# Kernel optimization log

Measured on AMD Instinct MI355X. Metric: run time of the kernel, lower is better.

The kernel has to match this reference:

```python
import jax, jax.numpy as jnp
import numpy as np

B, CIN, H, W = 2, 32, 64, 64
COUT, K, PAD = 32, 3, 1
KK = K * K
PRED_W = COUT * CIN * KK  # 9216 dynamic-weight channels
PRED_OUT = PRED_W + COUT  # + per-pixel bias
EPS = 1e-12


def setup_inputs() -> dict:
    key = jax.random.key(0)
    k1, k2 = jax.random.split(key)
    x = jax.random.normal(k1, (B, CIN, H, W), dtype=jnp.float32)
    # 1x1-conv predictor weights (Conv2d(in_ch, pred_out, 1)), fan-in scaled
    Wp = jax.random.normal(k2, (PRED_OUT, CIN), dtype=jnp.float32) / np.sqrt(CIN).astype(np.float32)
    bp = jnp.zeros((PRED_OUT,), dtype=jnp.float32)
    return {"x": x, "Wp": Wp, "bp": bp}


def _unfold3x3(x):
    # F.unfold with k=3, pad=1, stride=1, dilation=1 -> (B, Cin, 9, L), c slowest then (kh, kw)
    xp = jnp.pad(x, ((0, 0), (0, 0), (PAD, PAD), (PAD, PAD)))
    patches = jnp.stack(
        [xp[:, :, i:i + H, j:j + W] for i in range(K) for j in range(K)], axis=2
    )  # (B, Cin, 9, H, W)
    return patches.reshape(B, CIN, KK, H * W)


def _l2norm(v, axis):
    n = jnp.sqrt(jnp.sum(v * v, axis=axis, keepdims=True))
    return v / jnp.maximum(n, EPS)


def reference(x, Wp, bp):
    L = H * W
    patches = _unfold3x3(x)  # (B, Cin, 9, L)
    # 1x1 conv predictor (stride=1 path -> operates on x directly)
    pred = jnp.einsum('oc,bchw->bohw', Wp, x) + bp[None, :, None, None]  # (B, PRED_OUT, H, W)
    dyn_w = pred[:, :PRED_W].reshape(B, COUT, CIN, KK, L)
    dyn_b = pred[:, PRED_W:].reshape(B, COUT, L)
    # norm_pred: L2-normalize over Cin axis, then over k*k axis
    dyn_w = _l2norm(dyn_w, axis=2)
    dyn_w = _l2norm(dyn_w, axis=3)
    out = jnp.einsum('bockl,bckl->bol', dyn_w, patches) + dyn_b  # (B, Cout, L)
    return out.reshape(B, COUT, H, W)
```

## Files before the change

### kernel.cpp

```cpp
#include <hip/hip_runtime.h>

#define TPB 256

typedef __attribute__((ext_vector_type(8))) short short8;
typedef __attribute__((ext_vector_type(4))) float f32x4;

__device__ __forceinline__ unsigned f2bf_pk(float a, float b) {
  return ((__float_as_uint(a) + 0x8000u) >> 16) | ((__float_as_uint(b) + 0x8000u) & 0xffff0000u);
}
__device__ __forceinline__ float bflo(unsigned v) { return __uint_as_float(v << 16); }
__device__ __forceinline__ float bfhi(unsigned v) { return __uint_as_float(v & 0xffff0000u); }

__device__ __forceinline__ void dma16(const void* g, void* l) {
  __builtin_amdgcn_global_load_lds(
      (const __attribute__((address_space(1))) unsigned*)g,
      (__attribute__((address_space(3))) unsigned*)l, 16, 0, 0);
}

__global__ void prep_kernel(const float* __restrict__ Wp, unsigned* __restrict__ Wq) {
  int idx = blockIdx.x * blockDim.x + threadIdx.x;
  if (idx >= 32 * 18 * 64 * 4) return;
  int j2   = idx & 3;
  int lane = (idx >> 2) & 63;
  int rt   = (idx >> 8) % 18;
  int o    = (idx >> 8) / 18;
  int m16 = lane & 15, kq = lane >> 4;
  int row = o * 288 + (m16 >> 2) * 72 + rt * 4 + (m16 & 3);
  const float* src = Wp + row * 32 + kq * 8 + j2 * 2;
  Wq[idx] = f2bf_pk(src[0], src[1]);
}

template <bool USE_WQ>
__global__ __launch_bounds__(TPB, 2) void dppc8_kernel(
    const float* __restrict__ x, const float* __restrict__ Wp,
    const float* __restrict__ bp, const unsigned* __restrict__ Wq,
    float* __restrict__ out) {
  __shared__ __align__(16) unsigned short xrow2[3 * 66 * 40];
  __shared__ __align__(16) char wqbuf[2][18432];
  __shared__ __align__(16) float bp_s[4 * 288];
  __shared__ __align__(16) float Wb_s[4 * 32];
  __shared__ float bias4[4];

  const int tid = threadIdx.x;
  const int bid = blockIdx.x;
  const int og  = bid & 7;
  const int t   = bid >> 3;
  const int b   = t >> 6;
  const int h   = t & 63;

  const char* wq_g = (const char*)Wq + (size_t)(og * 4) * 18432;

  if (USE_WQ) {
    for (int c = tid; c < 1152; c += TPB)
      dma16(wq_g + c * 16, wqbuf[0] + c * 16);
  }

  for (int i = tid; i < 120; i += TPB) {
    int p = i / 20, w = i % 20;
    ((unsigned*)xrow2)[(((p >> 1) * 66 + ((p & 1) ? 65 : 0)) * 20) + w] = 0;
  }
  for (int i = tid; i < 1536; i += TPB) {
    int px_ = i & 63, c4 = (i >> 6) & 7, r = i >> 9;
    int hh = h - 1 + r;
    unsigned w0 = 0, w1 = 0;
    if ((unsigned)hh < 64u) {
      const float* xp = x + ((b * 32 + c4 * 4) * 64 + hh) * 64 + px_;
      float f0 = xp[0], f1 = xp[4096], f2 = xp[8192], f3 = xp[12288];
      w0 = f2bf_pk(f0, f1);
      w1 = f2bf_pk(f2, f3);
    }
    uint2* dst = (uint2*)&xrow2[(r * 66 + 1 + px_) * 40 + c4 * 4];
    *dst = make_uint2(w0, w1);
  }
  for (int i = tid; i < 1152; i += TPB) bp_s[i] = bp[og * 1152 + i];
  if (tid < 128) Wb_s[tid] = Wp[(9216 + og * 4 + (tid >> 5)) * 32 + (tid & 31)];
  if (tid < 4) bias4[tid] = bp[9216 + og * 4 + tid];
  __syncthreads();

  const int lane = tid & 63;
  const int wv   = tid >> 6;
  const int m16  = lane & 15, kq = lane >> 4;
  const int px   = wv * 16 + m16;

  const short8 bfrag = *(const short8*)&xrow2[(66 + 1 + px) * 40 + kq * 8];

  unsigned patch2[36];
#pragma unroll
  for (int kk = 0; kk < 9; ++kk) {
    const int kh = kk / 3, kw = kk - kh * 3;
    const uint4 tp = *(const uint4*)&xrow2[(kh * 66 + kw + px) * 40 + kq * 8];
    patch2[kk * 4 + 0] = tp.x;
    patch2[kk * 4 + 1] = tp.y;
    patch2[kk * 4 + 2] = tp.z;
    patch2[kk * 4 + 3] = tp.w;
  }

#pragma unroll 1
  for (int oo = 0; oo < 4; ++oo) {
    const int o = og * 4 + oo;
    const int buf = oo & 1;

    if (USE_WQ && oo < 3) {
      const char* g = wq_g + (size_t)(oo + 1) * 18432;
      for (int c = tid; c < 1152; c += TPB)
        dma16(g + c * 16, wqbuf[buf ^ 1] + c * 16);
    }

    f32x4 acc[18];
    if (USE_WQ) {
#pragma unroll
      for (int rt = 0; rt < 18; ++rt) {
        const short8 a = *(const short8*)(wqbuf[buf] + (rt * 64 + lane) * 16);
        const f32x4 bb = *(const f32x4*)&bp_s[oo * 288 + kq * 72 + rt * 4];
        acc[rt] = __builtin_amdgcn_mfma_f32_16x16x32_bf16(a, bfrag, bb, 0, 0, 0);
      }
    } else {
      const float* ab = Wp + (o * 288 + (m16 >> 2) * 72 + (m16 & 3)) * 32 + kq * 8;
#pragma unroll
      for (int rt = 0; rt < 18; ++rt) {
        const float* ap = ab + rt * 4 * 32;
        float4 a0 = *(const float4*)ap;
        float4 a1 = *(const float4*)(ap + 4);
        union { short8 v; unsigned u[4]; } af;
        af.u[0] = f2bf_pk(a0.x, a0.y);
        af.u[1] = f2bf_pk(a0.z, a0.w);
        af.u[2] = f2bf_pk(a1.x, a1.y);
        af.u[3] = f2bf_pk(a1.z, a1.w);
        const f32x4 bb = *(const f32x4*)&bp_s[oo * 288 + kq * 72 + rt * 4];
        acc[rt] = __builtin_amdgcn_mfma_f32_16x16x32_bf16(af.v, bfrag, bb, 0, 0, 0);
      }
    }

    float rinv[9];
#pragma unroll
    for (int kk = 0; kk < 9; ++kk) rinv[kk] = 0.f;
#pragma unroll
    for (int c8 = 0; c8 < 8; ++c8)
#pragma unroll
      for (int kk = 0; kk < 9; ++kk) {
        const int idx = c8 * 9 + kk;
        const float v = acc[idx >> 2][idx & 3];
        rinv[kk] += v * v;
      }
#pragma unroll
    for (int kk = 0; kk < 9; ++kk) {
      float s = rinv[kk];
      s += __shfl_xor(s, 16);
      s += __shfl_xor(s, 32);
      rinv[kk] = rsqrtf(fmaxf(s, 1e-24f));
    }

    float oacc = 0.f;
#pragma unroll
    for (int c8 = 0; c8 < 8; ++c8) {
      float s2 = 0.f, dot = 0.f;
#pragma unroll
      for (int kk = 0; kk < 9; ++kk) {
        const int idx = c8 * 9 + kk;
        const float tv = acc[idx >> 2][idx & 3] * rinv[kk];
        s2 += tv * tv;
        const unsigned wd = patch2[kk * 4 + (c8 >> 1)];
        const float pv = (c8 & 1) ? bfhi(wd) : bflo(wd);
        dot += tv * pv;
      }
      oacc += rsqrtf(fmaxf(s2, 1e-24f)) * dot;
      const unsigned wc = patch2[16 + (c8 >> 1)];
      const float xc = (c8 & 1) ? bfhi(wc) : bflo(wc);
      oacc += Wb_s[oo * 32 + kq * 8 + c8] * xc;
    }
    oacc += __shfl_xor(oacc, 16);
    oacc += __shfl_xor(oacc, 32);
    if (kq == 0)
      out[((b * 32 + o) * 64 + h) * 64 + px] = oacc + bias4[oo];

    if (oo < 3) __syncthreads();
  }
}

extern "C" void kernel_launch(void* const* d_in, const int* in_sizes, int n_in,
                              void* d_out, int out_size, void* d_ws, size_t ws_size,
                              hipStream_t stream) {
  const float* x  = (const float*)d_in[0];
  const float* Wp = (const float*)d_in[1];
  const float* bp = (const float*)d_in[2];
  float* out = (float*)d_out;
  const size_t wq_bytes = (size_t)32 * 18 * 64 * 8 * 2;
  if (ws_size >= wq_bytes) {
    prep_kernel<<<576, 256, 0, stream>>>(Wp, (unsigned*)d_ws);
    dppc8_kernel<true><<<1024, TPB, 0, stream>>>(x, Wp, bp, (const unsigned*)d_ws, out);
  } else {
    dppc8_kernel<false><<<1024, TPB, 0, stream>>>(x, Wp, bp, nullptr, out);
  }
}
```

Baseline: 82.76 us.

## Single-buffer weight LDS and reload patches per iteration to raise occupancy

Replaces the double-buffered weight tile in LDS with a single buffer, refilled after the MFMAs of each output channel finish. The 36-register patch array is dropped: patches are reloaded from LDS inside the normalization loop. Launch bounds go from 2 to 4 blocks per SM. The aim is lower LDS and register use so more blocks stay resident, at the cost of an extra barrier, exposed weight-load latency, and repeated LDS reads of the patches.

```diff
diff --git a/kernel.cpp b/kernel.cpp
--- a/kernel.cpp
+++ b/kernel.cpp
@@ -31,12 +31,12 @@
 }
 
 template <bool USE_WQ>
-__global__ __launch_bounds__(TPB, 2) void dppc8_kernel(
+__global__ __launch_bounds__(TPB, 4) void dppc9_kernel(
     const float* __restrict__ x, const float* __restrict__ Wp,
     const float* __restrict__ bp, const unsigned* __restrict__ Wq,
     float* __restrict__ out) {
   __shared__ __align__(16) unsigned short xrow2[3 * 66 * 40];
-  __shared__ __align__(16) char wqbuf[2][18432];
+  __shared__ __align__(16) char wqbuf[18432];
   __shared__ __align__(16) float bp_s[4 * 288];
   __shared__ __align__(16) float Wb_s[4 * 32];
   __shared__ float bias4[4];
@@ -52,7 +52,7 @@
 
   if (USE_WQ) {
     for (int c = tid; c < 1152; c += TPB)
-      dma16(wq_g + c * 16, wqbuf[0] + c * 16);
+      dma16(wq_g + c * 16, wqbuf + c * 16);
   }
 
   for (int i = tid; i < 120; i += TPB) {
@@ -82,35 +82,17 @@
   const int m16  = lane & 15, kq = lane >> 4;
   const int px   = wv * 16 + m16;
 
-  const short8 bfrag = *(const short8*)&xrow2[(66 + 1 + px) * 40 + kq * 8];
-
-  unsigned patch2[36];
-#pragma unroll
-  for (int kk = 0; kk < 9; ++kk) {
-    const int kh = kk / 3, kw = kk - kh * 3;
-    const uint4 tp = *(const uint4*)&xrow2[(kh * 66 + kw + px) * 40 + kq * 8];
-    patch2[kk * 4 + 0] = tp.x;
-    patch2[kk * 4 + 1] = tp.y;
-    patch2[kk * 4 + 2] = tp.z;
-    patch2[kk * 4 + 3] = tp.w;
-  }
-
 #pragma unroll 1
   for (int oo = 0; oo < 4; ++oo) {
     const int o = og * 4 + oo;
-    const int buf = oo & 1;
 
-    if (USE_WQ && oo < 3) {
-      const char* g = wq_g + (size_t)(oo + 1) * 18432;
-      for (int c = tid; c < 1152; c += TPB)
-        dma16(g + c * 16, wqbuf[buf ^ 1] + c * 16);
-    }
+    const short8 bfrag = *(const short8*)&xrow2[(66 + 1 + px) * 40 + kq * 8];
 
     f32x4 acc[18];
     if (USE_WQ) {
 #pragma unroll
       for (int rt = 0; rt < 18; ++rt) {
-        const short8 a = *(const short8*)(wqbuf[buf] + (rt * 64 + lane) * 16);
+        const short8 a = *(const short8*)(wqbuf + (rt * 64 + lane) * 16);
         const f32x4 bb = *(const f32x4*)&bp_s[oo * 288 + kq * 72 + rt * 4];
         acc[rt] = __builtin_amdgcn_mfma_f32_16x16x32_bf16(a, bfrag, bb, 0, 0, 0);
       }
@@ -129,6 +111,13 @@
         const f32x4 bb = *(const f32x4*)&bp_s[oo * 288 + kq * 72 + rt * 4];
         acc[rt] = __builtin_amdgcn_mfma_f32_16x16x32_bf16(af.v, bfrag, bb, 0, 0, 0);
       }
+    }
+
+    if (USE_WQ && oo < 3) {
+      __syncthreads();
+      const char* g = wq_g + (size_t)(oo + 1) * 18432;
+      for (int c = tid; c < 1152; c += TPB)
+        dma16(g + c * 16, wqbuf + c * 16);
     }
 
     float rinv[9];
@@ -150,22 +139,32 @@
       rinv[kk] = rsqrtf(fmaxf(s, 1e-24f));
     }
 
+    float s2[8], dot[8];
+#pragma unroll
+    for (int c8 = 0; c8 < 8; ++c8) { s2[c8] = 0.f; dot[c8] = 0.f; }
+#pragma unroll
+    for (int kk = 0; kk < 9; ++kk) {
+      const int kh = kk / 3, kw = kk - kh * 3;
+      const uint4 tp = *(const uint4*)&xrow2[(kh * 66 + kw + px) * 40 + kq * 8];
+      const float rv = rinv[kk];
+#pragma unroll
+      for (int c8 = 0; c8 < 8; ++c8) {
+        const int idx = c8 * 9 + kk;
+        const float tv = acc[idx >> 2][idx & 3] * rv;
+        s2[c8] += tv * tv;
+        const unsigned wd = ((const unsigned*)&tp)[c8 >> 1];
+        const float pv = (c8 & 1) ? bfhi(wd) : bflo(wd);
+        dot[c8] += tv * pv;
+      }
+    }
+
+    const uint4 tc = *(const uint4*)&xrow2[(66 + 1 + px) * 40 + kq * 8];
     float oacc = 0.f;
 #pragma unroll
     for (int c8 = 0; c8 < 8; ++c8) {
-      float s2 = 0.f, dot = 0.f;
-#pragma unroll
-      for (int kk = 0; kk < 9; ++kk) {
-        const int idx = c8 * 9 + kk;
-        const float tv = acc[idx >> 2][idx & 3] * rinv[kk];
-        s2 += tv * tv;
-        const unsigned wd = patch2[kk * 4 + (c8 >> 1)];
-        const float pv = (c8 & 1) ? bfhi(wd) : bflo(wd);
-        dot += tv * pv;
-      }
-      oacc += rsqrtf(fmaxf(s2, 1e-24f)) * dot;
-      const unsigned wc = patch2[16 + (c8 >> 1)];
-      const float xc = (c8 & 1) ? bfhi(wc) : bflo(wc);
+      oacc += rsqrtf(fmaxf(s2[c8], 1e-24f)) * dot[c8];
+      const unsigned wd = ((const unsigned*)&tc)[c8 >> 1];
+      const float xc = (c8 & 1) ? bfhi(wd) : bflo(wd);
       oacc += Wb_s[oo * 32 + kq * 8 + c8] * xc;
     }
     oacc += __shfl_xor(oacc, 16);
@@ -187,8 +186,8 @@
   const size_t wq_bytes = (size_t)32 * 18 * 64 * 8 * 2;
   if (ws_size >= wq_bytes) {
     prep_kernel<<<576, 256, 0, stream>>>(Wp, (unsigned*)d_ws);
-    dppc8_kernel<true><<<1024, TPB, 0, stream>>>(x, Wp, bp, (const unsigned*)d_ws, out);
+    dppc9_kernel<true><<<1024, TPB, 0, stream>>>(x, Wp, bp, (const unsigned*)d_ws, out);
   } else {
-    dppc8_kernel<false><<<1024, TPB, 0, stream>>>(x, Wp, bp, nullptr, out);
+    dppc9_kernel<false><<<1024, TPB, 0, stream>>>(x, Wp, bp, nullptr, out);
   }
 }
```

Result: faster. 80.62 us (median of 2 runs) (-2.6%).
